# Performance work log

Hardware: AMD Instinct MI355X
Metric: run time of the kernel (lower is better)

## Reference

```python
import jax, jax.numpy as jnp
import numpy as np

B, H, W, C = 32, 56, 56, 384
NH, WS, SS = 12, 7, 3
DH = C // NH
N = WS * WS
HID = 4 * C
SCALE = DH ** -0.5


def _make_attn_mask(h, w, ws, ss):
    img = np.zeros((h, w), dtype=np.float32)
    cnt = 0
    for hs in (slice(0, -ws), slice(-ws, -ss), slice(-ss, None)):
        for wsl in (slice(0, -ws), slice(-ws, -ss), slice(-ss, None)):
            img[hs, wsl] = cnt
            cnt += 1
    mw = img.reshape(h // ws, ws, w // ws, ws).transpose(0, 2, 1, 3).reshape(-1, ws * ws)
    diff = mw[:, None, :] - mw[:, :, None]  # (nW, n, n)
    return np.where(diff != 0, np.float32(-100.0), np.float32(0.0))


def _make_rel_pos_index(ws):
    coords = np.stack(np.meshgrid(np.arange(ws), np.arange(ws), indexing='ij')).reshape(2, -1)
    rel = (coords[:, :, None] - coords[:, None, :]).transpose(1, 2, 0)  # (n, n, 2)
    rel[..., 0] += ws - 1
    rel[..., 1] += ws - 1
    rel[..., 0] *= 2 * ws - 1
    return rel.sum(-1)  # (n, n)


ATTN_MASK = jnp.asarray(_make_attn_mask(H, W, WS, SS))          # (nW, n, n)
REL_IDX = jnp.asarray(_make_rel_pos_index(WS))                   # (n, n)


def layernorm(x, g, b, eps):
    mu = jnp.mean(x, axis=-1, keepdims=True)
    var = jnp.var(x, axis=-1, keepdims=True)
    return (x - mu) * jax.lax.rsqrt(var + eps) * g + b


def window_partition(x, ws):
    b, h, w, c = x.shape
    x = x.reshape(b, h // ws, ws, w // ws, ws, c)
    return x.transpose(0, 1, 3, 2, 4, 5).reshape(-1, ws, ws, c)


def window_reverse(windows, ws, h, w):
    b = windows.shape[0] // ((h // ws) * (w // ws))
    x = windows.reshape(b, h // ws, w // ws, ws, ws, -1)
    return x.transpose(0, 1, 3, 2, 4, 5).reshape(b, h, w, -1)


def setup_inputs() -> dict:
    key = jax.random.key(0)
    ks = jax.random.split(key, 8)
    d = {
        'x': jax.random.normal(ks[0], (B, H * W, C), dtype=jnp.float32),
        'ln1_g': jnp.ones((C,), jnp.float32), 'ln1_b': jnp.zeros((C,), jnp.float32),
        'qkv_w': jax.random.normal(ks[1], (C, 3 * C), jnp.float32) * 0.02,
        'qkv_b': jnp.zeros((3 * C,), jnp.float32),
        'proj_w': jax.random.normal(ks[2], (C, C), jnp.float32) * 0.02,
        'proj_b': jnp.zeros((C,), jnp.float32),
        'rpb_table': jax.random.normal(ks[3], ((2 * WS - 1) ** 2, NH), jnp.float32) * 0.02,
        'ln2_g': jnp.ones((C,), jnp.float32), 'ln2_b': jnp.zeros((C,), jnp.float32),
        'ffln_g': jnp.ones((C,), jnp.float32), 'ffln_b': jnp.zeros((C,), jnp.float32),
        'ff1_w': jax.random.normal(ks[4], (C, HID), jnp.float32) * 0.02,
        'ff1_b': jnp.zeros((HID,), jnp.float32),
        'ff2_w': jax.random.normal(ks[5], (HID, C), jnp.float32) * 0.02,
        'ff2_b': jnp.zeros((C,), jnp.float32),
    }
    return d


def reference(x, ln1_g, ln1_b, qkv_w, qkv_b, proj_w, proj_b, rpb_table,
              ln2_g, ln2_b, ffln_g, ffln_b, ff1_w, ff1_b, ff2_w, ff2_b):
    b = x.shape[0]
    shortcut = x
    xn = layernorm(x, ln1_g, ln1_b, 1e-5).reshape(b, H, W, C)
    shifted = jnp.roll(xn, shift=(-SS, -SS), axis=(1, 2))
    xw = window_partition(shifted, WS).reshape(-1, N, C)  # (b*nW, n, c)
    Bw = xw.shape[0]
    nW = Bw // b

    qkv = (xw @ qkv_w + qkv_b).reshape(Bw, N, 3, NH, DH).transpose(2, 0, 3, 1, 4)
    q, k, v = qkv[0], qkv[1], qkv[2]  # (Bw, nh, n, dh)
    dots = jnp.einsum('bhnd,bhmd->bhnm', q, k) * SCALE

    bias = rpb_table[REL_IDX.reshape(-1)].reshape(N, N, NH).transpose(2, 0, 1)  # (nh, n, n)
    attn = dots + bias[None]
    attn = attn.reshape(b, nW, NH, N, N) + ATTN_MASK[None, :, None, :, :]
    attn = jax.nn.softmax(attn.reshape(Bw, NH, N, N), axis=-1)

    out = jnp.einsum('bhnm,bhmd->bhnd', attn, v)
    out = out.transpose(0, 2, 1, 3).reshape(Bw, N, C)
    out = out @ proj_w + proj_b

    out = window_reverse(out.reshape(-1, WS, WS, C), WS, H, W)
    out = jnp.roll(out, shift=(SS, SS), axis=(1, 2)).reshape(b, H * W, C)

    x = shortcut + out
    y = layernorm(x, ln2_g, ln2_b, 1e-5)
    y = layernorm(y, ffln_g, ffln_b, 1e-6)
    y = jax.nn.gelu(y @ ff1_w + ff1_b, approximate=False) @ ff2_w + ff2_b
    return x + y
```

## Files before the change

### kernel.cpp

```cpp
#include <hip/hip_runtime.h>
#include <hip/hip_bf16.h>

typedef short bf16x8 __attribute__((ext_vector_type(8)));
typedef short short4v __attribute__((ext_vector_type(4)));
typedef float f32x4  __attribute__((ext_vector_type(4)));

static constexpr float SCALE = 0.17677669529663687f;

__device__ __forceinline__ void gload_lds16(const void* g, void* l) {
  __builtin_amdgcn_global_load_lds(
      (const __attribute__((address_space(1))) unsigned int*)g,
      (__attribute__((address_space(3))) unsigned int*)l, 16, 0, 0);
}

__device__ __forceinline__ size_t win_to_nat(int t) {
  int win = t / 49; int n = t - win * 49;
  int bb = win >> 6; int wimg = win & 63;
  int hb = wimg >> 3, wb = wimg & 7;
  int nr = n / 7, nc = n - nr * 7;
  int hh = hb * 7 + nr + 3; if (hh >= 56) hh -= 56;
  int ww = wb * 7 + nc + 3; if (ww >= 56) ww -= 56;
  return (size_t)bb * 3136 + (size_t)hh * 56 + ww;
}

__device__ __forceinline__ float gelu_fast(float x) {
  float t = __expf(-1.702f * x);
  return x / (1.f + t);
}

__global__ __launch_bounds__(256)
void k_transpose(const float* __restrict__ W, __hip_bfloat16* __restrict__ Wt,
                 int K, int N) {
  __shared__ float tile[32][33];
  int tx = threadIdx.x & 31, ty = threadIdx.x >> 5;
  int tc = blockIdx.x, tr = blockIdx.y;
#pragma unroll
  for (int r = 0; r < 32; r += 8)
    tile[r + ty][tx] = W[(size_t)(tr * 32 + r + ty) * N + tc * 32 + tx];
  __syncthreads();
#pragma unroll
  for (int r = 0; r < 32; r += 8)
    Wt[(size_t)(tc * 32 + r + ty) * K + tr * 32 + tx] =
        __float2bfloat16(tile[tx][r + ty]);
}

__global__ __launch_bounds__(256)
void k_ln1(const float* __restrict__ x, const float* __restrict__ gw,
           const float* __restrict__ bw, __hip_bfloat16* __restrict__ xw) {
  int lane = threadIdx.x & 63;
  int t = blockIdx.x * 4 + (threadIdx.x >> 6);
  size_t nt = win_to_nat(t);
  const float* xr = x + nt * 384;
  float4 a  = *(const float4*)(xr + lane * 4);
  float2 c2 = *(const float2*)(xr + 256 + lane * 2);
  float v[6] = {a.x, a.y, a.z, a.w, c2.x, c2.y};
  int c0 = lane * 4, c1 = 256 + lane * 2;
  int ch[6] = {c0, c0 + 1, c0 + 2, c0 + 3, c1, c1 + 1};
  float s = 0.f, q = 0.f;
#pragma unroll
  for (int i = 0; i < 6; i++) { s += v[i]; q += v[i] * v[i]; }
#pragma unroll
  for (int m = 1; m < 64; m <<= 1) { s += __shfl_xor(s, m); q += __shfl_xor(q, m); }
  float mean = s * (1.f / 384.f);
  float rstd = rsqrtf(q * (1.f / 384.f) - mean * mean + 1e-5f);
  __hip_bfloat16* o = xw + (size_t)t * 384;
#pragma unroll
  for (int i = 0; i < 6; i++)
    o[ch[i]] = __float2bfloat16((v[i] - mean) * rstd * gw[ch[i]] + bw[ch[i]]);
}

__global__ __launch_bounds__(256)
void k_ln2ff(const float* __restrict__ xres, const float* __restrict__ g2,
             const float* __restrict__ b2, const float* __restrict__ gf,
             const float* __restrict__ bf_, __hip_bfloat16* __restrict__ yln) {
  int lane = threadIdx.x & 63;
  int t = blockIdx.x * 4 + (threadIdx.x >> 6);
  const float* xr = xres + (size_t)t * 384;
  float4 a  = *(const float4*)(xr + lane * 4);
  float2 c2 = *(const float2*)(xr + 256 + lane * 2);
  float v[6] = {a.x, a.y, a.z, a.w, c2.x, c2.y};
  int c0 = lane * 4, c1 = 256 + lane * 2;
  int ch[6] = {c0, c0 + 1, c0 + 2, c0 + 3, c1, c1 + 1};
  float s = 0.f, q = 0.f;
#pragma unroll
  for (int i = 0; i < 6; i++) { s += v[i]; q += v[i] * v[i]; }
#pragma unroll
  for (int m = 1; m < 64; m <<= 1) { s += __shfl_xor(s, m); q += __shfl_xor(q, m); }
  float mean = s * (1.f / 384.f);
  float rstd = rsqrtf(q * (1.f / 384.f) - mean * mean + 1e-5f);
  float y1[6];
  s = 0.f; q = 0.f;
#pragma unroll
  for (int i = 0; i < 6; i++) {
    y1[i] = (v[i] - mean) * rstd * g2[ch[i]] + b2[ch[i]];
    s += y1[i]; q += y1[i] * y1[i];
  }
#pragma unroll
  for (int m = 1; m < 64; m <<= 1) { s += __shfl_xor(s, m); q += __shfl_xor(q, m); }
  float m2 = s * (1.f / 384.f);
  float r2 = rsqrtf(q * (1.f / 384.f) - m2 * m2 + 1e-6f);
  __hip_bfloat16* o = yln + (size_t)t * 384;
#pragma unroll
  for (int i = 0; i < 6; i++)
    o[ch[i]] = __float2bfloat16((y1[i] - m2) * r2 * gf[ch[i]] + bf_[ch[i]]);
}

enum { EPI_QKV = 0, EPI_PROJ = 1, EPI_FF1 = 2, EPI_FF2 = 3 };

template <int EPI>
__global__ __launch_bounds__(256)
void k_gemm(const __hip_bfloat16* __restrict__ A, const __hip_bfloat16* __restrict__ Wt,
            const float* __restrict__ bias, int K, int nCol, int cpx,
            const float* __restrict__ aux,
            float* __restrict__ out_f,
            __hip_bfloat16* __restrict__ out_b) {
  __shared__ __hip_bfloat16 LB[24576];
  int tid = threadIdx.x;
  int lane = tid & 63, w = tid >> 6;
  int g = lane >> 4, r16 = lane & 15;
  int wr = w >> 1, wc = w & 1;

  int bid = blockIdx.x;
  int wg = (bid & 7) * cpx + (bid >> 3);
  int rB = wg / nCol;
  int rowBlk = rB * 128;
  int colBlk = (wg - rB * nCol) * 128;

  int s2 = (tid & 7) ^ ((tid >> 3) & 7);
  int srow = 2 * (tid >> 3) + (s2 >> 2);
  int cch = s2 & 3;
  const __hip_bfloat16* PA = A + (size_t)(rowBlk + srow) * K + cch * 8;
  const __hip_bfloat16* PB = Wt + (size_t)(colBlk + srow) * K + cch * 8;

#define STG(NB, T)                                                            \
  {                                                                           \
    int k0s = (T) << 5;                                                       \
    _Pragma("unroll") for (int j = 0; j < 2; j++) {                           \
      gload_lds16(PA + (size_t)j * 64 * K + k0s, &LB[(NB) * 4096 + j * 2048 + w * 512]); \
      gload_lds16(PB + (size_t)j * 64 * K + k0s, &LB[12288 + (NB) * 4096 + j * 2048 + w * 512]); \
    }                                                                         \
  }

  int rslot = (g + ((r16 & 1) << 2)) ^ (r16 >> 1);
  int aBase = (wr * 32 + (r16 >> 1)) * 64 + rslot * 8;
  int bBase = 12288 + (wc * 32 + (r16 >> 1)) * 64 + rslot * 8;

  f32x4 acc[4][4] = {};
  const int nt = K >> 5;

  STG(0, 0)
  STG(1, 1)

#define STEP(CB, SB, T)                                                       \
  {                                                                           \
    if ((T) + 2 < nt) {                                                       \
      STG(SB, (T) + 2)                                                        \
      asm volatile("s_waitcnt vmcnt(8)" ::: "memory");                        \
    } else if ((T) + 1 < nt) {                                                \
      asm volatile("s_waitcnt vmcnt(4)" ::: "memory");                        \
    } else {                                                                  \
      asm volatile("s_waitcnt vmcnt(0)" ::: "memory");                        \
    }                                                                         \
    __builtin_amdgcn_s_barrier();                \
    bf16x8 a[4], b[4];                                                        \
    _Pragma("unroll") for (int mi = 0; mi < 4; mi++)                          \
      a[mi] = *(const bf16x8*)(&LB[(CB) * 4096 + aBase + mi * 512]);          \
    _Pragma("unroll") for (int ni = 0; ni < 4; ni++)                          \
      b[ni] = *(const bf16x8*)(&LB[(CB) * 4096 + bBase + ni * 512]);          \
    __builtin_amdgcn_s_setprio(1);                                            \
    _Pragma("unroll") for (int mi = 0; mi < 4; mi++)                          \
      _Pragma("unroll") for (int ni = 0; ni < 4; ni++)                        \
        acc[mi][ni] = __builtin_amdgcn_mfma_f32_16x16x32_bf16(                \
            b[ni], a[mi], acc[mi][ni], 0, 0, 0);                              \
    __builtin_amdgcn_s_setprio(0);                                            \
    __builtin_amdgcn_s_barrier();     \
  }

  for (int t = 0; t < nt; t += 3) {
    STEP(0, 2, t)
    STEP(1, 0, t + 1)
    STEP(2, 1, t + 2)
  }
#undef STEP
#undef STG

  if constexpr (EPI == EPI_QKV || EPI == EPI_FF1) {
    __hip_bfloat16* EP = &LB[w * 4096];
#pragma unroll
    for (int ni = 0; ni < 4; ni++) {
      float4 b4 = *(const float4*)(bias + colBlk + wc * 64 + ni * 16 + g * 4);
#pragma unroll
      for (int mi = 0; mi < 4; mi++) {
        float v0 = acc[mi][ni][0] + b4.x, v1 = acc[mi][ni][1] + b4.y,
              v2 = acc[mi][ni][2] + b4.z, v3 = acc[mi][ni][3] + b4.w;
        if constexpr (EPI == EPI_FF1) {
          v0 = gelu_fast(v0); v1 = gelu_fast(v1);
          v2 = gelu_fast(v2); v3 = gelu_fast(v3);
        }
        short4v s4 = {(short)__bfloat16_as_ushort(__float2bfloat16(v0)),
                      (short)__bfloat16_as_ushort(__float2bfloat16(v1)),
                      (short)__bfloat16_as_ushort(__float2bfloat16(v2)),
                      (short)__bfloat16_as_ushort(__float2bfloat16(v3))};
        int row = mi * 16 + r16;
        int ch8 = (ni * 2 + (g >> 1)) ^ (row & 7);
        *(short4v*)(&EP[row * 64 + ch8 * 8 + (g & 1) * 4]) = s4;
      }
    }
#pragma unroll
    for (int j = 0; j < 8; j++) {
      int r = j * 8 + (lane >> 3);
      bf16x8 vv = *(const bf16x8*)(&EP[r * 64 + ((lane & 7) ^ (r & 7)) * 8]);
      int grow = rowBlk + wr * 64 + r;
      int col0 = colBlk + wc * 64 + (lane & 7) * 8;
      if constexpr (EPI == EPI_QKV) {
        int winr = grow / 49, nn = grow - winr * 49;
        int which = col0 / 384; int rem = col0 - which * 384;
        int hh = rem >> 5, dd = rem & 31;
        size_t off = (((size_t)winr * 12 + hh) * 49 + nn) * 32 + dd;
        *(bf16x8*)(out_b + (size_t)which * 38535168u + off) = vv;
      } else {
        *(bf16x8*)(out_b + (size_t)grow * 1536 + col0) = vv;
      }
    }
  } else {
    float* EPF = (float*)LB + w * 2048;
#pragma unroll
    for (int half = 0; half < 2; half++) {
#pragma unroll
      for (int ni = 0; ni < 4; ni++) {
        float4 b4 = *(const float4*)(bias + colBlk + wc * 64 + ni * 16 + g * 4);
#pragma unroll
        for (int mi2 = 0; mi2 < 2; mi2++) {
          int mi = half * 2 + mi2;
          f32x4 v = acc[mi][ni];
          v[0] += b4.x; v[1] += b4.y; v[2] += b4.z; v[3] += b4.w;
          int row = mi2 * 16 + r16;
          int ch4 = (ni * 4 + g) ^ r16;
          *(f32x4*)(&EPF[row * 64 + ch4 * 4]) = v;
        }
      }
#pragma unroll
      for (int j = 0; j < 8; j++) {
        int r = j * 4 + g;
        f32x4 vv = *(const f32x4*)(&EPF[r * 64 + ((r16 ^ (r & 15)) * 4)]);
        int grow = rowBlk + wr * 64 + half * 32 + r;
        int col0 = colBlk + wc * 64 + r16 * 4;
        if constexpr (EPI == EPI_PROJ) {
          size_t nt2 = win_to_nat(grow);
          const float4 a4 = *(const float4*)(aux + nt2 * 384 + col0);
          float4 o4 = {vv[0] + a4.x, vv[1] + a4.y, vv[2] + a4.z, vv[3] + a4.w};
          *(float4*)(out_f + nt2 * 384 + col0) = o4;
        } else {
          const float4 a4 = *(const float4*)(aux + (size_t)grow * 384 + col0);
          float4 o4 = {vv[0] + a4.x, vv[1] + a4.y, vv[2] + a4.z, vv[3] + a4.w};
          *(float4*)(out_f + (size_t)grow * 384 + col0) = o4;
        }
      }
    }
  }
}

__global__ __launch_bounds__(256)
void k_attn(const __hip_bfloat16* __restrict__ q, const __hip_bfloat16* __restrict__ k,
            const __hip_bfloat16* __restrict__ v, const float* __restrict__ rpb,
            __hip_bfloat16* __restrict__ o) {
  __shared__ __hip_bfloat16 P[4][64][72];
  int tid = threadIdx.x;
  int lane = tid & 63, wave = tid >> 6;
  int g = lane >> 4, r16 = lane & 15;
  int gid = blockIdx.x * 4 + wave;
  int wi = gid / 12, h = gid - (gid / 12) * 12;
  int wimg = wi & 63;
  int hb = wimg >> 3, wb = wimg & 7;
  size_t base = ((size_t)wi * 12 + h) * (49 * 32);
  const __hip_bfloat16* qb = q + base;
  const __hip_bfloat16* kb = k + base;
  const __hip_bfloat16* vb = v + base;

  bf16x8 zf = {0, 0, 0, 0, 0, 0, 0, 0};
  bf16x8 qf[4], kf[4];
#pragma unroll
  for (int mi = 0; mi < 4; mi++) {
    int row = mi * 16 + r16;
    qf[mi] = (row < 49) ? *(const bf16x8*)(qb + row * 32 + g * 8) : zf;
    kf[mi] = (row < 49) ? *(const bf16x8*)(kb + row * 32 + g * 8) : zf;
  }
  f32x4 fz = {0.f, 0.f, 0.f, 0.f};
  f32x4 S[4][4];
#pragma unroll
  for (int mi = 0; mi < 4; mi++)
#pragma unroll
    for (int ni = 0; ni < 4; ni++)
      S[mi][ni] = __builtin_amdgcn_mfma_f32_16x16x32_bf16(qf[mi], kf[ni], fz, 0, 0, 0);

  int kiA[4], kjA[4], rkA[4], cvA[4];
#pragma unroll
  for (int ni = 0; ni < 4; ni++) {
    int col = ni * 16 + r16;
    cvA[ni] = (col < 49);
    int ki = col / 7, kj = col - (col / 7) * 7;
    kiA[ni] = ki; kjA[ni] = kj;
    int hg = hb * 7 + ki, wg = wb * 7 + kj;
    int rh = (hg < 49) ? 0 : ((hg < 53) ? 1 : 2);
    int rw = (wg < 49) ? 0 : ((wg < 53) ? 1 : 2);
    rkA[ni] = rh * 3 + rw;
  }

#pragma unroll
  for (int mi = 0; mi < 4; mi++) {
#pragma unroll
    for (int rr = 0; rr < 4; rr++) {
      int row = mi * 16 + g * 4 + rr;
      float sv[4];
      float mx = -1e30f;
      int qi = row / 7, qj = row - (row / 7) * 7;
      int hgq = hb * 7 + qi, wgq = wb * 7 + qj;
      int rhq = (hgq < 49) ? 0 : ((hgq < 53) ? 1 : 2);
      int rwq = (wgq < 49) ? 0 : ((wgq < 53) ? 1 : 2);
      int rq = rhq * 3 + rwq;
#pragma unroll
      for (int ni = 0; ni < 4; ni++) {
        float s = -1e30f;
        if (row < 49 && cvA[ni]) {
          int idx = (qi - kiA[ni] + 6) * 13 + (qj - kjA[ni] + 6);
          float maskv = (rq != rkA[ni]) ? -100.f : 0.f;
          s = S[mi][ni][rr] * SCALE + rpb[idx * 12 + h] + maskv;
        }
        sv[ni] = s;
        mx = fmaxf(mx, s);
      }
#pragma unroll
      for (int m = 1; m <= 8; m <<= 1) mx = fmaxf(mx, __shfl_xor(mx, m));
      float sum = 0.f;
#pragma unroll
      for (int ni = 0; ni < 4; ni++) {
        float p = __expf(sv[ni] - mx);
        sv[ni] = p; sum += p;
      }
#pragma unroll
      for (int m = 1; m <= 8; m <<= 1) sum += __shfl_xor(sum, m);
      float inv = 1.f / sum;
#pragma unroll
      for (int ni = 0; ni < 4; ni++)
        P[wave][row][ni * 16 + r16] = __float2bfloat16(sv[ni] * inv);
    }
  }

  f32x4 O[4][2] = {};
#pragma unroll
  for (int ks = 0; ks < 2; ks++) {
    bf16x8 pf[4];
#pragma unroll
    for (int mi = 0; mi < 4; mi++)
      pf[mi] = *(const bf16x8*)(&P[wave][mi * 16 + r16][ks * 32 + g * 8]);
#pragma unroll
    for (int ni = 0; ni < 2; ni++) {
      bf16x8 vf = zf;
#pragma unroll
      for (int j = 0; j < 8; j++) {
        int m = ks * 32 + g * 8 + j;
        if (m < 49) vf[j] = ((const short*)vb)[m * 32 + ni * 16 + r16];
      }
#pragma unroll
      for (int mi = 0; mi < 4; mi++)
        O[mi][ni] = __builtin_amdgcn_mfma_f32_16x16x32_bf16(pf[mi], vf, O[mi][ni], 0, 0, 0);
    }
  }

#pragma unroll
  for (int mi = 0; mi < 4; mi++)
#pragma unroll
    for (int rr = 0; rr < 4; rr++) {
      int row = mi * 16 + g * 4 + rr;
      if (row < 49) {
#pragma unroll
        for (int ni = 0; ni < 2; ni++) {
          int col = ni * 16 + r16;
          o[(((size_t)wi * 49 + row) * 12 + h) * 32 + col] = __float2bfloat16(O[mi][ni][rr]);
        }
      }
    }
}

extern "C" void kernel_launch(void* const* d_in, const int* in_sizes, int n_in,
                              void* d_out, int out_size, void* d_ws, size_t ws_size,
                              hipStream_t stream) {
  const float* x      = (const float*)d_in[0];
  const float* ln1_g  = (const float*)d_in[1];
  const float* ln1_b  = (const float*)d_in[2];
  const float* qkv_w  = (const float*)d_in[3];
  const float* qkv_b  = (const float*)d_in[4];
  const float* proj_w = (const float*)d_in[5];
  const float* proj_b = (const float*)d_in[6];
  const float* rpb    = (const float*)d_in[7];
  const float* ln2_g  = (const float*)d_in[8];
  const float* ln2_b  = (const float*)d_in[9];
  const float* ffg    = (const float*)d_in[10];
  const float* ffb    = (const float*)d_in[11];
  const float* ff1_w  = (const float*)d_in[12];
  const float* ff1_b  = (const float*)d_in[13];
  const float* ff2_w  = (const float*)d_in[14];
  const float* ff2_b  = (const float*)d_in[15];
  float* out = (float*)d_out;

  char* ws = (char*)d_ws;
  __hip_bfloat16* xw     = (__hip_bfloat16*)ws;
  __hip_bfloat16* qbuf   = (__hip_bfloat16*)(ws + 77070336u);
  __hip_bfloat16* kbuf   = qbuf + 38535168u;
  __hip_bfloat16* vbuf   = kbuf + 38535168u;
  __hip_bfloat16* attn_o = xw;
  __hip_bfloat16* hbuf   = (__hip_bfloat16*)ws;
  float*          x_res  = (float*)(ws + 308281344u);
  __hip_bfloat16* yln    = (__hip_bfloat16*)(ws + 462422016u);
  __hip_bfloat16* qkv_wt = (__hip_bfloat16*)(ws + 539492352u);
  __hip_bfloat16* proj_wt = qkv_wt + 442368u;
  __hip_bfloat16* ff1_wt  = proj_wt + 147456u;
  __hip_bfloat16* ff2_wt  = ff1_wt + 589824u;

  k_transpose<<<dim3(1152 / 32, 384 / 32), dim3(256), 0, stream>>>(qkv_w, qkv_wt, 384, 1152);
  k_transpose<<<dim3(384 / 32, 384 / 32), dim3(256), 0, stream>>>(proj_w, proj_wt, 384, 384);
  k_transpose<<<dim3(1536 / 32, 384 / 32), dim3(256), 0, stream>>>(ff1_w, ff1_wt, 384, 1536);
  k_transpose<<<dim3(384 / 32, 1536 / 32), dim3(256), 0, stream>>>(ff2_w, ff2_wt, 1536, 384);

  k_ln1<<<dim3(25088), dim3(256), 0, stream>>>(x, ln1_g, ln1_b, xw);

  k_gemm<EPI_QKV><<<dim3(7056), dim3(256), 0, stream>>>(xw, qkv_wt, qkv_b, 384, 9, 7056 / 8,
                                                        nullptr, nullptr, qbuf);
  k_attn<<<dim3(6144), dim3(256), 0, stream>>>(qbuf, kbuf, vbuf, rpb, attn_o);
  k_gemm<EPI_PROJ><<<dim3(2352), dim3(256), 0, stream>>>(attn_o, proj_wt, proj_b, 384, 3, 2352 / 8,
                                                         x, x_res, nullptr);
  k_ln2ff<<<dim3(25088), dim3(256), 0, stream>>>(x_res, ln2_g, ln2_b, ffg, ffb, yln);
  k_gemm<EPI_FF1><<<dim3(9408), dim3(256), 0, stream>>>(yln, ff1_wt, ff1_b, 384, 12, 9408 / 8,
                                                        nullptr, nullptr, hbuf);
  k_gemm<EPI_FF2><<<dim3(2352), dim3(256), 0, stream>>>(hbuf, ff2_wt, ff2_b, 1536, 3, 2352 / 8,
                                                        x_res, out, nullptr);
}
```

Baseline: 901.0 us.

## Enlarge GEMM tiles to 256x192 with 512-thread blocks and single-barrier pipeline

Switches the GEMM from 128x128 tiles with 4 waves to 256x192 tiles with 8 waves. Each wave now holds a 4x6 MFMA accumulator block, which raises arithmetic intensity and cuts redundant A/B loads from global memory. The triple-buffered pipeline drops its trailing barrier and issues the next stage's async loads after the LDS fragment reads. The epilogue is rebuilt as a phased, shared staging pass through LDS for coalesced stores. In exchange it uses more LDS and registers per block, and with fewer blocks the CUs may be less evenly filled.

```diff
diff --git a/kernel.cpp b/kernel.cpp
--- a/kernel.cpp
+++ b/kernel.cpp
@@ -108,13 +108,13 @@
 enum { EPI_QKV = 0, EPI_PROJ = 1, EPI_FF1 = 2, EPI_FF2 = 3 };
 
 template <int EPI>
-__global__ __launch_bounds__(256)
+__global__ __launch_bounds__(512, 2)
 void k_gemm(const __hip_bfloat16* __restrict__ A, const __hip_bfloat16* __restrict__ Wt,
             const float* __restrict__ bias, int K, int nCol, int cpx,
             const float* __restrict__ aux,
             float* __restrict__ out_f,
             __hip_bfloat16* __restrict__ out_b) {
-  __shared__ __hip_bfloat16 LB[24576];
+  __shared__ __hip_bfloat16 LB[43008];
   int tid = threadIdx.x;
   int lane = tid & 63, w = tid >> 6;
   int g = lane >> 4, r16 = lane & 15;
@@ -123,29 +123,31 @@
   int bid = blockIdx.x;
   int wg = (bid & 7) * cpx + (bid >> 3);
   int rB = wg / nCol;
-  int rowBlk = rB * 128;
-  int colBlk = (wg - rB * nCol) * 128;
+  int rowBlk = rB * 256;
+  int colBlk = (wg - rB * nCol) * 192;
 
   int s2 = (tid & 7) ^ ((tid >> 3) & 7);
   int srow = 2 * (tid >> 3) + (s2 >> 2);
   int cch = s2 & 3;
   const __hip_bfloat16* PA = A + (size_t)(rowBlk + srow) * K + cch * 8;
   const __hip_bfloat16* PB = Wt + (size_t)(colBlk + srow) * K + cch * 8;
+  size_t K128 = (size_t)128 * K;
 
 #define STG(NB, T)                                                            \
   {                                                                           \
     int k0s = (T) << 5;                                                       \
-    _Pragma("unroll") for (int j = 0; j < 2; j++) {                           \
-      gload_lds16(PA + (size_t)j * 64 * K + k0s, &LB[(NB) * 4096 + j * 2048 + w * 512]); \
-      gload_lds16(PB + (size_t)j * 64 * K + k0s, &LB[12288 + (NB) * 4096 + j * 2048 + w * 512]); \
-    }                                                                         \
+    gload_lds16(PA + k0s,        &LB[(NB) * 8192 + w * 512]);                 \
+    gload_lds16(PA + K128 + k0s, &LB[(NB) * 8192 + 4096 + w * 512]);          \
+    gload_lds16(PB + k0s,        &LB[24576 + (NB) * 6144 + w * 512]);         \
+    if (tid < 256)                                                            \
+      gload_lds16(PB + K128 + k0s, &LB[24576 + (NB) * 6144 + 4096 + w * 512]);\
   }
 
   int rslot = (g + ((r16 & 1) << 2)) ^ (r16 >> 1);
   int aBase = (wr * 32 + (r16 >> 1)) * 64 + rslot * 8;
-  int bBase = 12288 + (wc * 32 + (r16 >> 1)) * 64 + rslot * 8;
-
-  f32x4 acc[4][4] = {};
+  int bOff  = (wc * 48 + (r16 >> 1)) * 64 + rslot * 8;
+
+  f32x4 acc[4][6] = {};
   const int nt = K >> 5;
 
   STG(0, 0)
@@ -153,27 +155,26 @@
 
 #define STEP(CB, SB, T)                                                       \
   {                                                                           \
-    if ((T) + 2 < nt) {                                                       \
-      STG(SB, (T) + 2)                                                        \
-      asm volatile("s_waitcnt vmcnt(8)" ::: "memory");                        \
-    } else if ((T) + 1 < nt) {                                                \
-      asm volatile("s_waitcnt vmcnt(4)" ::: "memory");                        \
+    if ((T) < nt - 1) {                                                       \
+      if (w < 4) asm volatile("s_waitcnt vmcnt(4)" ::: "memory");             \
+      else       asm volatile("s_waitcnt vmcnt(3)" ::: "memory");             \
     } else {                                                                  \
       asm volatile("s_waitcnt vmcnt(0)" ::: "memory");                        \
     }                                                                         \
-    __builtin_amdgcn_s_barrier();                \
-    bf16x8 a[4], b[4];                                                        \
+    __builtin_amdgcn_s_barrier();                                             \
+    asm volatile("" ::: "memory");                                            \
+    bf16x8 a[4], b[6];                                                        \
     _Pragma("unroll") for (int mi = 0; mi < 4; mi++)                          \
-      a[mi] = *(const bf16x8*)(&LB[(CB) * 4096 + aBase + mi * 512]);          \
-    _Pragma("unroll") for (int ni = 0; ni < 4; ni++)                          \
-      b[ni] = *(const bf16x8*)(&LB[(CB) * 4096 + bBase + ni * 512]);          \
+      a[mi] = *(const bf16x8*)(&LB[(CB) * 8192 + aBase + mi * 512]);          \
+    _Pragma("unroll") for (int ni = 0; ni < 6; ni++)                          \
+      b[ni] = *(const bf16x8*)(&LB[24576 + (CB) * 6144 + bOff + ni * 512]);   \
+    if ((T) + 2 < nt) STG(SB, (T) + 2)                                        \
     __builtin_amdgcn_s_setprio(1);                                            \
     _Pragma("unroll") for (int mi = 0; mi < 4; mi++)                          \
-      _Pragma("unroll") for (int ni = 0; ni < 4; ni++)                        \
+      _Pragma("unroll") for (int ni = 0; ni < 6; ni++)                        \
         acc[mi][ni] = __builtin_amdgcn_mfma_f32_16x16x32_bf16(                \
             b[ni], a[mi], acc[mi][ni], 0, 0, 0);                              \
     __builtin_amdgcn_s_setprio(0);                                            \
-    __builtin_amdgcn_s_barrier();     \
   }
 
   for (int t = 0; t < nt; t += 3) {
@@ -185,66 +186,77 @@
 #undef STG
 
   if constexpr (EPI == EPI_QKV || EPI == EPI_FF1) {
-    __hip_bfloat16* EP = &LB[w * 4096];
-#pragma unroll
-    for (int ni = 0; ni < 4; ni++) {
-      float4 b4 = *(const float4*)(bias + colBlk + wc * 64 + ni * 16 + g * 4);
-#pragma unroll
-      for (int mi = 0; mi < 4; mi++) {
-        float v0 = acc[mi][ni][0] + b4.x, v1 = acc[mi][ni][1] + b4.y,
-              v2 = acc[mi][ni][2] + b4.z, v3 = acc[mi][ni][3] + b4.w;
-        if constexpr (EPI == EPI_FF1) {
-          v0 = gelu_fast(v0); v1 = gelu_fast(v1);
-          v2 = gelu_fast(v2); v3 = gelu_fast(v3);
-        }
-        short4v s4 = {(short)__bfloat16_as_ushort(__float2bfloat16(v0)),
-                      (short)__bfloat16_as_ushort(__float2bfloat16(v1)),
-                      (short)__bfloat16_as_ushort(__float2bfloat16(v2)),
-                      (short)__bfloat16_as_ushort(__float2bfloat16(v3))};
-        int row = mi * 16 + r16;
-        int ch8 = (ni * 2 + (g >> 1)) ^ (row & 7);
-        *(short4v*)(&EP[row * 64 + ch8 * 8 + (g & 1) * 4]) = s4;
-      }
-    }
-#pragma unroll
-    for (int j = 0; j < 8; j++) {
-      int r = j * 8 + (lane >> 3);
-      bf16x8 vv = *(const bf16x8*)(&EP[r * 64 + ((lane & 7) ^ (r & 7)) * 8]);
-      int grow = rowBlk + wr * 64 + r;
-      int col0 = colBlk + wc * 64 + (lane & 7) * 8;
-      if constexpr (EPI == EPI_QKV) {
-        int winr = grow / 49, nn = grow - winr * 49;
-        int which = col0 / 384; int rem = col0 - which * 384;
-        int hh = rem >> 5, dd = rem & 31;
-        size_t off = (((size_t)winr * 12 + hh) * 49 + nn) * 32 + dd;
-        *(bf16x8*)(out_b + (size_t)which * 38535168u + off) = vv;
-      } else {
-        *(bf16x8*)(out_b + (size_t)grow * 1536 + col0) = vv;
+    __hip_bfloat16* EP = LB;
+#pragma unroll
+    for (int p = 0; p < 2; p++) {
+      __builtin_amdgcn_s_barrier();
+      if ((wr >> 1) == p) {
+        int rw = (wr & 1) * 64;
+#pragma unroll
+        for (int ni = 0; ni < 6; ni++) {
+          float4 b4 = *(const float4*)(bias + colBlk + wc * 96 + ni * 16 + g * 4);
+#pragma unroll
+          for (int mi = 0; mi < 4; mi++) {
+            float v0 = acc[mi][ni][0] + b4.x, v1 = acc[mi][ni][1] + b4.y,
+                  v2 = acc[mi][ni][2] + b4.z, v3 = acc[mi][ni][3] + b4.w;
+            if constexpr (EPI == EPI_FF1) {
+              v0 = gelu_fast(v0); v1 = gelu_fast(v1);
+              v2 = gelu_fast(v2); v3 = gelu_fast(v3);
+            }
+            short4v s4 = {(short)__bfloat16_as_ushort(__float2bfloat16(v0)),
+                          (short)__bfloat16_as_ushort(__float2bfloat16(v1)),
+                          (short)__bfloat16_as_ushort(__float2bfloat16(v2)),
+                          (short)__bfloat16_as_ushort(__float2bfloat16(v3))};
+            int r = rw + mi * 16 + r16;
+            *(short4v*)(&EP[r * 200 + wc * 96 + ni * 16 + g * 4]) = s4;
+          }
+        }
+      }
+      __builtin_amdgcn_s_barrier();
+#pragma unroll
+      for (int i = 0; i < 6; i++) {
+        int idx = i * 512 + tid;
+        int row = idx / 24, cc = idx - row * 24;
+        bf16x8 vv = *(const bf16x8*)(&EP[row * 200 + cc * 8]);
+        int grow = rowBlk + p * 128 + row;
+        int col0 = colBlk + cc * 8;
+        if constexpr (EPI == EPI_QKV) {
+          int winr = grow / 49, nn = grow - winr * 49;
+          int which = col0 / 384; int rem = col0 - which * 384;
+          int hh = rem >> 5, dd = rem & 31;
+          size_t off = (((size_t)winr * 12 + hh) * 49 + nn) * 32 + dd;
+          *(bf16x8*)(out_b + (size_t)which * 38535168u + off) = vv;
+        } else {
+          *(bf16x8*)(out_b + (size_t)grow * 1536 + col0) = vv;
+        }
       }
     }
   } else {
-    float* EPF = (float*)LB + w * 2048;
-#pragma unroll
-    for (int half = 0; half < 2; half++) {
-#pragma unroll
-      for (int ni = 0; ni < 4; ni++) {
-        float4 b4 = *(const float4*)(bias + colBlk + wc * 64 + ni * 16 + g * 4);
-#pragma unroll
-        for (int mi2 = 0; mi2 < 2; mi2++) {
-          int mi = half * 2 + mi2;
-          f32x4 v = acc[mi][ni];
-          v[0] += b4.x; v[1] += b4.y; v[2] += b4.z; v[3] += b4.w;
-          int row = mi2 * 16 + r16;
-          int ch4 = (ni * 4 + g) ^ r16;
-          *(f32x4*)(&EPF[row * 64 + ch4 * 4]) = v;
-        }
-      }
-#pragma unroll
-      for (int j = 0; j < 8; j++) {
-        int r = j * 4 + g;
-        f32x4 vv = *(const f32x4*)(&EPF[r * 64 + ((r16 ^ (r & 15)) * 4)]);
-        int grow = rowBlk + wr * 64 + half * 32 + r;
-        int col0 = colBlk + wc * 64 + r16 * 4;
+    float* EPF = (float*)LB;
+#pragma unroll
+    for (int q = 0; q < 4; q++) {
+      __builtin_amdgcn_s_barrier();
+      if (wr == q) {
+#pragma unroll
+        for (int ni = 0; ni < 6; ni++) {
+          float4 b4 = *(const float4*)(bias + colBlk + wc * 96 + ni * 16 + g * 4);
+#pragma unroll
+          for (int mi = 0; mi < 4; mi++) {
+            f32x4 v = acc[mi][ni];
+            v[0] += b4.x; v[1] += b4.y; v[2] += b4.z; v[3] += b4.w;
+            int r = mi * 16 + r16;
+            *(f32x4*)(&EPF[r * 200 + wc * 96 + ni * 16 + g * 4]) = v;
+          }
+        }
+      }
+      __builtin_amdgcn_s_barrier();
+#pragma unroll
+      for (int i = 0; i < 6; i++) {
+        int idx = i * 512 + tid;
+        int row = idx / 48, cc = idx - row * 48;
+        f32x4 vv = *(const f32x4*)(&EPF[row * 200 + cc * 4]);
+        int grow = rowBlk + q * 64 + row;
+        int col0 = colBlk + cc * 4;
         if constexpr (EPI == EPI_PROJ) {
           size_t nt2 = win_to_nat(grow);
           const float4 a4 = *(const float4*)(aux + nt2 * 384 + col0);
@@ -424,14 +436,14 @@
 
   k_ln1<<<dim3(25088), dim3(256), 0, stream>>>(x, ln1_g, ln1_b, xw);
 
-  k_gemm<EPI_QKV><<<dim3(7056), dim3(256), 0, stream>>>(xw, qkv_wt, qkv_b, 384, 9, 7056 / 8,
+  k_gemm<EPI_QKV><<<dim3(2352), dim3(512), 0, stream>>>(xw, qkv_wt, qkv_b, 384, 6, 2352 / 8,
                                                         nullptr, nullptr, qbuf);
   k_attn<<<dim3(6144), dim3(256), 0, stream>>>(qbuf, kbuf, vbuf, rpb, attn_o);
-  k_gemm<EPI_PROJ><<<dim3(2352), dim3(256), 0, stream>>>(attn_o, proj_wt, proj_b, 384, 3, 2352 / 8,
-                                                         x, x_res, nullptr);
+  k_gemm<EPI_PROJ><<<dim3(784), dim3(512), 0, stream>>>(attn_o, proj_wt, proj_b, 384, 2, 784 / 8,
+                                                        x, x_res, nullptr);
   k_ln2ff<<<dim3(25088), dim3(256), 0, stream>>>(x_res, ln2_g, ln2_b, ffg, ffb, yln);
-  k_gemm<EPI_FF1><<<dim3(9408), dim3(256), 0, stream>>>(yln, ff1_wt, ff1_b, 384, 12, 9408 / 8,
+  k_gemm<EPI_FF1><<<dim3(3136), dim3(512), 0, stream>>>(yln, ff1_wt, ff1_b, 384, 8, 3136 / 8,
                                                         nullptr, nullptr, hbuf);
-  k_gemm<EPI_FF2><<<dim3(2352), dim3(256), 0, stream>>>(hbuf, ff2_wt, ff2_b, 1536, 3, 2352 / 8,
-                                                        x_res, out, nullptr);
-}
+  k_gemm<EPI_FF2><<<dim3(784), dim3(512), 0, stream>>>(hbuf, ff2_wt, ff2_b, 1536, 2, 784 / 8,
+                                                       x_res, out, nullptr);
+}
```

Result: slower. 1.003 ms (+11.3%).
